# Performance work log

Measured on AMD Instinct MI355X. Metric: run time of the kernel, lower is better.

The kernel has to match this reference:

```python
import jax, jax.numpy as jnp
import numpy as np
import math

B, N, DEG, C, F0, NCLS = 128, 512, 8, 128, 128, 10
E = B * N * DEG
RATIO = 0.8
K1 = math.ceil(RATIO * N)    # 410
K2 = math.ceil(RATIO * K1)   # 328
K3 = math.ceil(RATIO * K2)   # 263


def setup_inputs() -> dict:
    key = jax.random.key(0)
    ks = jax.random.split(key, 32)
    x = jax.random.normal(ks[0], (B * N, F0), jnp.float32)
    epg = N * DEG
    src_l = jax.random.randint(ks[1], (B, epg), 0, N)
    dst_l = jax.random.randint(ks[2], (B, epg), 0, N)
    off = (jnp.arange(B, dtype=jnp.int32) * N)[:, None]
    edge_src = (src_l + off).reshape(-1).astype(jnp.int32)
    edge_dst = (dst_l + off).reshape(-1).astype(jnp.int32)

    def lin(k, fi, fo):
        return jax.random.normal(k, (fi, fo), jnp.float32) / np.float32(np.sqrt(fi))

    inp = {"x": x, "edge_src": edge_src, "edge_dst": edge_dst}
    i = 3
    for s, fi in (("1", F0), ("2", C), ("3", C)):
        inp["Wroot" + s] = lin(ks[i], fi, C); i += 1
        inp["Wrel" + s] = lin(ks[i], fi, C); i += 1
        inp["brel" + s] = jnp.zeros((C,), jnp.float32)
        inp["p" + s] = jax.random.normal(ks[i], (C,), jnp.float32); i += 1
    inp["W1"] = lin(ks[i], 2 * C, 128); i += 1
    inp["b1"] = jnp.zeros((128,), jnp.float32)
    inp["W2"] = lin(ks[i], 128, 64); i += 1
    inp["b2"] = jnp.zeros((64,), jnp.float32)
    inp["W3"] = lin(ks[i], 64, NCLS); i += 1
    inp["b3"] = jnp.zeros((NCLS,), jnp.float32)
    return inp


def graph_conv(x, src, dst, emask, Wroot, Wrel, brel, num_nodes):
    # PyG GraphConv (aggr='add'): lin_rel(sum_j x_j) + lin_root(x_i)
    msg = x[src] * emask[:, None]                      # masked gather  [E, C]
    agg = jax.ops.segment_sum(msg, dst, num_segments=num_nodes)
    return agg @ Wrel + brel + x @ Wroot


def topk_pool(x, p, src, dst, emask, b, n, k):
    # score = tanh(x . p / ||p||), keep top-k nodes per graph, scale kept x by score
    score = jnp.tanh((x @ p) / jnp.linalg.norm(p))     # [b*n]
    vals, idx = jax.lax.top_k(score.reshape(b, n), k)  # [b, k]
    perm = (idx + (jnp.arange(b, dtype=idx.dtype) * n)[:, None]).reshape(-1)
    x_new = x[perm] * vals.reshape(-1, 1)
    inv = jnp.full((b * n,), -1, jnp.int32).at[perm].set(
        jnp.arange(b * k, dtype=jnp.int32))
    ns, nd = inv[src], inv[dst]
    nmask = emask * (ns >= 0) * (nd >= 0)
    return x_new, jnp.maximum(ns, 0), jnp.maximum(nd, 0), nmask


def readout(h, b, k):
    hb = h.reshape(b, k, -1)
    return jnp.concatenate([hb.max(axis=1), hb.mean(axis=1)], axis=-1)  # gmp||gap


def reference(x, edge_src, edge_dst,
              Wroot1, Wrel1, brel1, p1,
              Wroot2, Wrel2, brel2, p2,
              Wroot3, Wrel3, brel3, p3,
              W1, b1, W2, b2, W3, b3):
    emask = jnp.ones((E,), x.dtype)
    s, d = edge_src, edge_dst

    h = jax.nn.relu(graph_conv(x, s, d, emask, Wroot1, Wrel1, brel1, B * N))
    h, s, d, emask = topk_pool(h, p1, s, d, emask, B, N, K1)
    x1 = readout(h, B, K1)

    h = jax.nn.relu(graph_conv(h, s, d, emask, Wroot2, Wrel2, brel2, B * K1))
    h, s, d, emask = topk_pool(h, p2, s, d, emask, B, K1, K2)
    x2 = readout(h, B, K2)

    h = jax.nn.relu(graph_conv(h, s, d, emask, Wroot3, Wrel3, brel3, B * K2))
    h, s, d, emask = topk_pool(h, p3, s, d, emask, B, K2, K3)
    x3 = readout(h, B, K3)

    g = x1 + x2 + x3                                   # [B, 256]
    g = jax.nn.relu(g @ W1 + b1)                       # dropout is identity in eval
    g = jax.nn.relu(g @ W2 + b2)
    return jax.nn.log_softmax(g @ W3 + b3, axis=-1)    # [B, NCLS]
```

## Files before the change

### kernel.cpp

```cpp
#include <hip/hip_runtime.h>
#include <hip/hip_bf16.h>
#include <math.h>

#define B_G   128
#define N0    512
#define DEG   8
#define CCH   128
#define EPG   (N0*DEG)
#define E_TOTAL (B_G*EPG)
#define K1    410
#define K2    328
#define K3    263
#define NCLS  10

#define SWZ(row, cb) ((((cb) ^ ((row) & 7)) << 2))

using bf16x8 = __attribute__((ext_vector_type(8))) __bf16;
using f32x4  = __attribute__((ext_vector_type(4))) float;
typedef unsigned short ushort;
typedef unsigned int uint;
typedef unsigned long long u64;

__device__ __forceinline__ ushort f2b(float f) {
    uint u = __float_as_uint(f);
    u += 0x7fffu + ((u >> 16) & 1u);
    return (ushort)(u >> 16);
}
__device__ __forceinline__ float b2f(ushort h) {
    return __uint_as_float(((uint)h) << 16);
}
__device__ __forceinline__ void split2(float v, ushort& hi, ushort& lo) {
    hi = f2b(v);
    lo = f2b(v - b2f(hi));
}
__device__ __forceinline__ uint pksplit(float v) {
    ushort h, l; split2(v, h, l);
    return (uint)h | ((uint)l << 16);
}
__device__ __forceinline__ float unpk(uint u) {
    return __uint_as_float(u << 16) + __uint_as_float(u & 0xffff0000u);
}
__device__ __forceinline__ float keyval(u64 key) {
    uint tu = (uint)(key >> 32);
    uint su = (tu & 0x80000000u) ? (tu & 0x7fffffffu) : ~tu;
    return __uint_as_float(su);
}

__global__ __launch_bounds__(512) void setup_kernel(
        const float* __restrict__ Wrel0, const float* __restrict__ Wroot0,
        const float* __restrict__ Wrel1, const float* __restrict__ Wroot1,
        const float* __restrict__ Wrel2, const float* __restrict__ Wroot2,
        ushort* __restrict__ Bph, ushort* __restrict__ Bpl,
        const int* __restrict__ es, const int* __restrict__ ed,
        int* __restrict__ indptr0, int* __restrict__ counts0, ushort* __restrict__ srclist0) {
    __shared__ uint epk[EPG];
    __shared__ int cnt[512], pref[512], curs[512];
    if (blockIdx.x < B_G) {
        int b = blockIdx.x, tid = threadIdx.x;
        cnt[tid] = 0;
        __syncthreads();
        int base = b * EPG;
        for (int i = tid; i < EPG; i += 512) {
            int s = es[base + i] & (N0 - 1);
            int d = ed[base + i] & (N0 - 1);
            epk[i] = (uint)s | ((uint)d << 16);
            atomicAdd(&cnt[d], 1);
        }
        __syncthreads();
        pref[tid] = cnt[tid];
        __syncthreads();
        for (int off = 1; off < 512; off <<= 1) {
            int v = (tid >= off) ? pref[tid - off] : 0;
            __syncthreads();
            pref[tid] += v;
            __syncthreads();
        }
        int excl = tid ? pref[tid - 1] : 0;
        indptr0[b * N0 + tid] = base + excl;
        counts0[b * N0 + tid] = cnt[tid];
        curs[tid] = excl;
        __syncthreads();
        for (int i = tid; i < EPG; i += 512) {
            uint wv = epk[i];
            int dl = wv >> 16;
            int pos = atomicAdd(&curs[dl], 1);
            srclist0[base + pos] = (ushort)(wv & 0xFFFFu);
        }
    } else {
        int i = (blockIdx.x - B_G) * 512 + threadIdx.x;
        if (i < 3 * 32768) {
            int layer = i >> 15, rem = i & 32767;
            int j = rem & 7, lane = (rem >> 3) & 63, cf = (rem >> 9) & 7, ks = rem >> 12;
            int k = ks * 32 + (lane >> 4) * 8 + j;
            int c = cf * 16 + (lane & 15);
            const float* Wrel  = layer == 0 ? Wrel0  : layer == 1 ? Wrel1  : Wrel2;
            const float* Wroot = layer == 0 ? Wroot0 : layer == 1 ? Wroot1 : Wroot2;
            float v = (k < 128) ? Wrel[k * 128 + c] : Wroot[(k - 128) * 128 + c];
            ushort hi, lo; split2(v, hi, lo);
            Bph[i] = hi; Bpl[i] = lo;
        }
    }
}

__global__ __launch_bounds__(1024) void aggregate0(
        const float* __restrict__ xf,
        const int* __restrict__ indptr, const int* __restrict__ counts,
        const ushort* __restrict__ srclist,
        uint* __restrict__ aggp) {
    extern __shared__ float slab[];
    int b = blockIdx.x >> 2, q = blockIdx.x & 3;
    int tid = threadIdx.x;
    const float4* xf4 = (const float4*)xf;
    for (int t = tid; t < N0 * 8; t += 1024) {
        int nd = t >> 3, c4 = t & 7;
        float4 u = xf4[(size_t)(b * N0 + nd) * 32 + q * 8 + c4];
        *(float4*)&slab[nd * 32 + SWZ(nd, c4)] = u;
    }
    __syncthreads();
    int wave = tid >> 6, lane = tid & 63;
    int gl = lane >> 3, sub = lane & 7;
    for (int g = wave; g < N0 / 8; g += 16) {
        int d = g * 8 + gl;
        int beg = indptr[b * N0 + d];
        int cnt = counts[b * N0 + d];
        float4 acc = make_float4(0.f, 0.f, 0.f, 0.f);
        int id_next = (cnt > 0) ? (int)srclist[beg] : 0;
        for (int j = 0; j < cnt; j++) {
            int id = id_next;
            if (j + 1 < cnt) id_next = (int)srclist[beg + j + 1];
            const float4 v = *(const float4*)&slab[id * 32 + SWZ(id, sub)];
            acc.x += v.x; acc.y += v.y; acc.z += v.z; acc.w += v.w;
        }
        uint4 o;
        o.x = pksplit(acc.x); o.y = pksplit(acc.y);
        o.z = pksplit(acc.z); o.w = pksplit(acc.w);
        *(uint4*)&aggp[(size_t)(b * N0 + d) * CCH + q * 32 + sub * 4] = o;
    }
}

__global__ __launch_bounds__(512, 4) void transform_mfma(
        const uint* __restrict__ aggp, const uint* __restrict__ rootp,
        const float* __restrict__ rootf,
        const ushort* __restrict__ Bph, const ushort* __restrict__ Bpl,
        const float* __restrict__ brel, const float* __restrict__ pvec,
        uint* __restrict__ hout, float* __restrict__ score) {
    __shared__ ushort ldsBh[16384];
    __shared__ ushort ldsBl[16384];
    int tid = threadIdx.x;
    int wave = tid >> 6, lane = tid & 63;
    int r = lane & 15, kb = lane >> 4;
    int rows0 = blockIdx.x * 128 + wave * 16;
    int gid = rows0 + r;

    f32x4 acc[8];
#pragma unroll
    for (int cf = 0; cf < 8; cf++) acc[cf] = (f32x4)(0.f);

    union U16 { uint u[4]; bf16x8 v; };

#pragma unroll
    for (int half = 0; half < 2; half++) {
        if (half) __syncthreads();
#pragma unroll
        for (int i = 0; i < 4; i++) {
            int idx = tid + i * 512;
            ((uint4*)ldsBh)[idx] = ((const uint4*)(Bph + half * 16384))[idx];
            ((uint4*)ldsBl)[idx] = ((const uint4*)(Bpl + half * 16384))[idx];
        }
        __syncthreads();
#pragma unroll
        for (int ks4 = 0; ks4 < 4; ks4++) {
            U16 ah, al;
            if (half && rootf) {
                const float* R = rootf + (size_t)gid * CCH + ks4 * 32 + kb * 8;
                float4 f0 = *(const float4*)R;
                float4 f1 = *(const float4*)(R + 4);
                float c[8] = {f0.x, f0.y, f0.z, f0.w, f1.x, f1.y, f1.z, f1.w};
#pragma unroll
                for (int p2 = 0; p2 < 4; p2++) {
                    ushort h0, l0, h1, l1;
                    split2(c[2 * p2], h0, l0);
                    split2(c[2 * p2 + 1], h1, l1);
                    ah.u[p2] = (uint)h0 | ((uint)h1 << 16);
                    al.u[p2] = (uint)l0 | ((uint)l1 << 16);
                }
            } else {
                const uint* A = half ? rootp : aggp;
                size_t rowbase = (size_t)gid * CCH + ks4 * 32 + kb * 8;
                uint4 ua = *(const uint4*)&A[rowbase];
                uint4 ub = *(const uint4*)&A[rowbase + 4];
                ah.u[0] = (ua.x & 0xffffu) | (ua.y << 16);
                ah.u[1] = (ua.z & 0xffffu) | (ua.w << 16);
                ah.u[2] = (ub.x & 0xffffu) | (ub.y << 16);
                ah.u[3] = (ub.z & 0xffffu) | (ub.w << 16);
                al.u[0] = (ua.x >> 16) | (ua.y & 0xffff0000u);
                al.u[1] = (ua.z >> 16) | (ua.w & 0xffff0000u);
                al.u[2] = (ub.x >> 16) | (ub.y & 0xffff0000u);
                al.u[3] = (ub.z >> 16) | (ub.w & 0xffff0000u);
            }
#pragma unroll
            for (int cf = 0; cf < 8; cf++) {
                bf16x8 bh = *(const bf16x8*)&ldsBh[((ks4 * 8 + cf) * 64 + lane) * 8];
                bf16x8 bl = *(const bf16x8*)&ldsBl[((ks4 * 8 + cf) * 64 + lane) * 8];
                acc[cf] = __builtin_amdgcn_mfma_f32_16x16x32_bf16(ah.v, bl, acc[cf], 0, 0, 0);
                acc[cf] = __builtin_amdgcn_mfma_f32_16x16x32_bf16(al.v, bh, acc[cf], 0, 0, 0);
                acc[cf] = __builtin_amdgcn_mfma_f32_16x16x32_bf16(ah.v, bh, acc[cf], 0, 0, 0);
            }
        }
    }

    float pv[8], bb[8], q = 0.f;
#pragma unroll
    for (int cf = 0; cf < 8; cf++) {
        pv[cf] = pvec[cf * 16 + r];
        bb[cf] = brel[cf * 16 + r];
        q += pv[cf] * pv[cf];
    }
    float dots[4] = {0.f, 0.f, 0.f, 0.f};
#pragma unroll
    for (int cf = 0; cf < 8; cf++) {
#pragma unroll
        for (int reg = 0; reg < 4; reg++) {
            float v = acc[cf][reg] + bb[cf];
            v = v > 0.f ? v : 0.f;
            hout[(size_t)(rows0 + kb * 4 + reg) * CCH + cf * 16 + r] = pksplit(v);
            dots[reg] += v * pv[cf];
        }
    }
#pragma unroll
    for (int off = 1; off < 16; off <<= 1) {
        q += __shfl_xor(q, off);
#pragma unroll
        for (int reg = 0; reg < 4; reg++) dots[reg] += __shfl_xor(dots[reg], off);
    }
    if (r == 0) {
        float inv_norm = rsqrtf(q);
#pragma unroll
        for (int reg = 0; reg < 4; reg++)
            score[rows0 + kb * 4 + reg] = tanhf(dots[reg] * inv_norm);
    }
}

__global__ __launch_bounds__(1024) void pool_kernel(
        const float* __restrict__ score, const uint* __restrict__ hp,
        float* __restrict__ gpart,
        const int* __restrict__ ipt_in, const int* __restrict__ cnt_in,
        const ushort* __restrict__ src_in,
        int* __restrict__ ipt_out, int* __restrict__ cnt_out,
        ushort* __restrict__ src_out,
        uint* __restrict__ pooledX, uint* __restrict__ aggout,
        int n, int k, int do_next) {
    int b = blockIdx.x >> 2, q = blockIdx.x & 3;
    int tid = threadIdx.x;
    __shared__ short invl[512];
    __shared__ short old_of[512];
    __shared__ float sval[512];
    __shared__ int hist[256];
    __shared__ int cum[257];
    __shared__ int bc[1];
    __shared__ float redbuf[1024];
    __shared__ int prefL[512];
    __shared__ int wtot[8], woff[8];
    extern __shared__ float slab[];

    u64 key = 0ull;
    bool has = (tid < n);
    if (has) {
        uint u = __float_as_uint(score[b * n + tid]);
        u = (u & 0x80000000u) ? ~u : (u | 0x80000000u);
        key = ((u64)u << 32) | (uint)(~tid);
        sval[tid] = keyval(key);
    }
    for (int t = tid; t < n * 8; t += 1024) {
        int nd = t >> 3, c4 = t & 7;
        uint4 u = *(const uint4*)&hp[(size_t)(b * n + nd) * CCH + q * 32 + c4 * 4];
        *(float4*)&slab[nd * 32 + SWZ(nd, c4)] =
            make_float4(unpk(u.x), unpk(u.y), unpk(u.z), unpk(u.w));
    }
    bool active = has, sure = false;
    int rem = k;
    for (int pass = 0; pass < 8; pass++) {
        int dig = (int)((key >> (56 - 8 * pass)) & 255);
        if (tid < 256) hist[tid] = 0;
        __syncthreads();
        if (active) atomicAdd(&hist[dig], 1);
        __syncthreads();
        if (tid < 64) {
            int b0 = hist[tid * 4], b1 = hist[tid * 4 + 1];
            int b2 = hist[tid * 4 + 2], b3 = hist[tid * 4 + 3];
            int s = b0 + b1 + b2 + b3;
            int suf = s;
#pragma unroll
            for (int o = 1; o < 64; o <<= 1) {
                int t2 = __shfl_down(suf, o);
                if (tid + o < 64) suf += t2;
            }
            int after = suf - s;
            cum[tid * 4 + 3] = after + b3;
            cum[tid * 4 + 2] = after + b3 + b2;
            cum[tid * 4 + 1] = after + b3 + b2 + b1;
            cum[tid * 4 + 0] = after + s;
            if (tid == 0) cum[256] = 0;
        }
        __syncthreads();
        if (tid < 256 && cum[tid] >= rem && cum[tid + 1] < rem) bc[0] = tid;
        __syncthreads();
        int dstar = bc[0];
        int hcnt = hist[dstar];
        rem -= cum[dstar + 1];
        if (active) {
            if (dig > dstar) { sure = true; active = false; }
            else if (dig < dstar) active = false;
        }
        __syncthreads();
        if (hcnt == 1) break;
    }
    bool sel = sure || (active && rem > 0);
    {
        int lane = tid & 63;
        int v = sel ? 1 : 0;
        int incl = v;
#pragma unroll
        for (int o = 1; o < 64; o <<= 1) {
            int t2 = __shfl_up(incl, o);
            if (lane >= o) incl += t2;
        }
        if (tid < 512 && lane == 63) wtot[tid >> 6] = incl;
        __syncthreads();
        if (tid < 8) {
            int s = 0;
            for (int w = 0; w < tid; w++) s += wtot[w];
            woff[tid] = s;
        }
        __syncthreads();
        if (tid < 512) {
            int rank = incl - v + woff[tid >> 6];
            invl[tid] = sel ? (short)rank : (short)-1;
            if (sel) old_of[rank] = (short)tid;
        }
        __syncthreads();
    }
    for (int t = tid; t < n * 8; t += 1024) {
        int nd = t >> 3, c4 = t & 7;
        if (invl[nd] >= 0) {
            float v = sval[nd];
            float* p = &slab[nd * 32 + SWZ(nd, c4)];
            p[0] *= v; p[1] *= v; p[2] *= v; p[3] *= v;
        }
    }
    __syncthreads();
    if (tid < 512) {
        int w = tid >> 5, ch = tid & 31;
        int cb = ch >> 2, ce = ch & 3;
        float mx = -1e30f, sm = 0.f;
        for (int nd = w; nd < n; nd += 16) {
            float v = slab[nd * 32 + SWZ(nd, cb) + ce];
            if (invl[nd] >= 0) { mx = fmaxf(mx, v); sm += v; }
        }
        redbuf[w * 32 + ch] = mx;
        redbuf[512 + w * 32 + ch] = sm;
    }
    __syncthreads();
    if (tid < 32) {
        float m = -1e30f, s = 0.f;
        for (int w = 0; w < 16; w++) {
            m = fmaxf(m, redbuf[w * 32 + tid]);
            s += redbuf[512 + w * 32 + tid];
        }
        gpart[b * 256 + q * 32 + tid] = m;
        gpart[b * 256 + 128 + q * 32 + tid] = s / (float)k;
    }
    if (!do_next) return;
    for (int t = tid; t < k * 8; t += 1024) {
        int rank = t >> 3, c4 = t & 7;
        int old = (int)old_of[rank];
        const float* p = &slab[old * 32 + SWZ(old, c4)];
        uint4 o;
        o.x = pksplit(p[0]); o.y = pksplit(p[1]);
        o.z = pksplit(p[2]); o.w = pksplit(p[3]);
        *(uint4*)&pooledX[(size_t)(b * k + rank) * CCH + q * 32 + c4 * 4] = o;
    }
    {
        int wave = tid >> 6, lane = tid & 63;
        int gl = lane >> 3, sub = lane & 7;
        int ngroups = (k + 7) >> 3;
        for (int g = wave; g < ngroups; g += 16) {
            int d = g * 8 + gl;
            bool act = d < k;
            int beg = 0, cc = 0;
            if (act) {
                int old = (int)old_of[d];
                beg = ipt_in[b * n + old];
                cc = cnt_in[b * n + old];
            }
            float4 acc = make_float4(0.f, 0.f, 0.f, 0.f);
            int s_next = (cc > 0) ? (int)src_in[beg] : 0;
            for (int j = 0; j < cc; j++) {
                int s = s_next;
                if (j + 1 < cc) s_next = (int)src_in[beg + j + 1];
                if (invl[s] >= 0) {
                    const float4 v = *(const float4*)&slab[s * 32 + SWZ(s, sub)];
                    acc.x += v.x; acc.y += v.y; acc.z += v.z; acc.w += v.w;
                }
            }
            if (act) {
                uint4 o;
                o.x = pksplit(acc.x); o.y = pksplit(acc.y);
                o.z = pksplit(acc.z); o.w = pksplit(acc.w);
                *(uint4*)&aggout[(size_t)(b * k + d) * CCH + q * 32 + sub * 4] = o;
            }
        }
    }
    if (q == 0) {
        int beg = 0, c = 0, nk = 0;
        if (tid < k) {
            int old = (int)old_of[tid];
            beg = ipt_in[b * n + old];
            c = cnt_in[b * n + old];
            for (int t = 0; t < c; t++)
                if (invl[src_in[beg + t]] >= 0) nk++;
        }
        int lane = tid & 63;
        int incl = (tid < 512 && tid < k) ? nk : 0;
#pragma unroll
        for (int o = 1; o < 64; o <<= 1) {
            int t2 = __shfl_up(incl, o);
            if (lane >= o) incl += t2;
        }
        if (tid < 512 && lane == 63) wtot[tid >> 6] = incl;
        __syncthreads();
        if (tid < 8) {
            int s = 0;
            for (int w = 0; w < tid; w++) s += wtot[w];
            woff[tid] = s;
        }
        __syncthreads();
        if (tid < 512) prefL[tid] = incl + woff[tid >> 6];
        __syncthreads();
        if (tid < k) {
            int excl = tid ? prefL[tid - 1] : 0;
            ipt_out[b * k + tid] = b * EPG + excl;
            cnt_out[b * k + tid] = nk;
            int pos = b * EPG + excl;
            for (int t = 0; t < c; t++) {
                int ns = invl[src_in[beg + t]];
                if (ns >= 0) src_out[pos++] = (ushort)ns;
            }
        }
    }
}

__global__ __launch_bounds__(128) void mlp_kernel(const float* __restrict__ gpart,
        const float* __restrict__ W1, const float* __restrict__ b1,
        const float* __restrict__ W2, const float* __restrict__ b2,
        const float* __restrict__ W3, const float* __restrict__ b3,
        float* __restrict__ out) {
    int b = blockIdx.x, t = threadIdx.x;
    __shared__ float gs[256], h1[128], h2[64], lg[10];
    const float* g0 = gpart + ((size_t)0 * B_G + b) * 256;
    const float* g1 = gpart + ((size_t)1 * B_G + b) * 256;
    const float* g2 = gpart + ((size_t)2 * B_G + b) * 256;
    gs[t] = g0[t] + g1[t] + g2[t];
    gs[128 + t] = g0[128 + t] + g1[128 + t] + g2[128 + t];
    __syncthreads();
    {
        float a = b1[t];
        for (int c = 0; c < 256; c++) a += gs[c] * W1[c * 128 + t];
        h1[t] = fmaxf(a, 0.f);
    }
    __syncthreads();
    if (t < 64) {
        float a = b2[t];
        for (int c = 0; c < 128; c++) a += h1[c] * W2[c * 64 + t];
        h2[t] = fmaxf(a, 0.f);
    }
    __syncthreads();
    if (t < 10) {
        float a = b3[t];
        for (int c = 0; c < 64; c++) a += h2[c] * W3[c * 10 + t];
        lg[t] = a;
    }
    __syncthreads();
    if (t < 10) {
        float m = lg[0];
        for (int i = 1; i < 10; i++) m = fmaxf(m, lg[i]);
        float s = 0.f;
        for (int i = 0; i < 10; i++) s += expf(lg[i] - m);
        out[b * 10 + t] = lg[t] - m - logf(s);
    }
}

extern "C" void kernel_launch(void* const* d_in, const int* in_sizes, int n_in,
                              void* d_out, int out_size, void* d_ws, size_t ws_size,
                              hipStream_t stream) {
    (void)in_sizes; (void)n_in; (void)out_size; (void)ws_size;
    const float* x0 = (const float*)d_in[0];
    const int* es = (const int*)d_in[1];
    const int* ed = (const int*)d_in[2];
    const float* Wroot[3] = {(const float*)d_in[3], (const float*)d_in[7], (const float*)d_in[11]};
    const float* Wrel[3]  = {(const float*)d_in[4], (const float*)d_in[8], (const float*)d_in[12]};
    const float* brel[3]  = {(const float*)d_in[5], (const float*)d_in[9], (const float*)d_in[13]};
    const float* pvec[3]  = {(const float*)d_in[6], (const float*)d_in[10], (const float*)d_in[14]};
    const float* W1 = (const float*)d_in[15];
    const float* b1 = (const float*)d_in[16];
    const float* W2 = (const float*)d_in[17];
    const float* b2 = (const float*)d_in[18];
    const float* W3 = (const float*)d_in[19];
    const float* b3 = (const float*)d_in[20];

    size_t off = 0;
    char* base = (char*)d_ws;
    auto alloc = [&](size_t bytes) -> void* {
        void* p = base + off;
        off += (bytes + 255) & ~(size_t)255;
        return p;
    };
    const size_t FEATP = (size_t)(B_G * N0) * CCH * 4;
    uint* P0 = (uint*)alloc(FEATP);
    uint* P1 = (uint*)alloc(FEATP);
    uint* P2 = (uint*)alloc(FEATP);
    ushort* Bph = (ushort*)alloc((size_t)3 * 32768 * 2);
    ushort* Bpl = (ushort*)alloc((size_t)3 * 32768 * 2);
    int* iptA = (int*)alloc((size_t)(B_G * N0) * 4);
    int* cntA = (int*)alloc((size_t)(B_G * N0) * 4);
    ushort* srcA = (ushort*)alloc((size_t)E_TOTAL * 2);
    int* iptB = (int*)alloc((size_t)(B_G * N0) * 4);
    int* cntB = (int*)alloc((size_t)(B_G * N0) * 4);
    ushort* srcB = (ushort*)alloc((size_t)E_TOTAL * 2);
    float* score = (float*)alloc((size_t)(B_G * N0) * 4);
    float* gpart = (float*)alloc((size_t)3 * B_G * 256 * 4);

    setup_kernel<<<B_G + (3 * 32768 + 511) / 512, 512, 0, stream>>>(
        Wrel[0], Wroot[0], Wrel[1], Wroot[1], Wrel[2], Wroot[2],
        Bph, Bpl, es, ed, iptA, cntA, srcA);

    aggregate0<<<4 * B_G, 1024, (size_t)N0 * 32 * 4, stream>>>(
        x0, iptA, cntA, srcA, P1);
    transform_mfma<<<B_G * N0 / 128, 512, 0, stream>>>(
        P1, nullptr, x0, Bph, Bpl, brel[0], pvec[0], P0, score);
    pool_kernel<<<4 * B_G, 1024, (size_t)N0 * 32 * 4, stream>>>(
        score, P0, gpart + (size_t)0 * B_G * 256,
        iptA, cntA, srcA, iptB, cntB, srcB, P2, P1, N0, K1, 1);

    transform_mfma<<<B_G * K1 / 128, 512, 0, stream>>>(
        P1, P2, nullptr, Bph + 32768, Bpl + 32768, brel[1], pvec[1], P0, score);
    pool_kernel<<<4 * B_G, 1024, (size_t)K1 * 32 * 4, stream>>>(
        score, P0, gpart + (size_t)1 * B_G * 256,
        iptB, cntB, srcB, iptA, cntA, srcA, P2, P1, K1, K2, 1);

    transform_mfma<<<B_G * K2 / 128, 512, 0, stream>>>(
        P1, P2, nullptr, Bph + 2 * 32768, Bpl + 2 * 32768, brel[2], pvec[2], P0, score);
    pool_kernel<<<4 * B_G, 1024, (size_t)K2 * 32 * 4, stream>>>(
        score, P0, gpart + (size_t)2 * B_G * 256,
        iptA, cntA, srcA, nullptr, nullptr, nullptr, nullptr, nullptr, K2, K3, 0);

    mlp_kernel<<<B_G, 128, 0, stream>>>(gpart, W1, b1, W2, b2, W3, b3, (float*)d_out);
}
```

Measured before the change: 199.6 us.

## Replace per-stage graph compaction with validity masks over the fixed node layout

After: 194.2 us (median of 2 runs). 2.7% less time.

```diff
diff --git a/kernel.cpp b/kernel.cpp
--- a/kernel.cpp
+++ b/kernel.cpp
@@ -242,42 +242,41 @@
 }
 
 __global__ __launch_bounds__(1024) void pool_kernel(
-        const float* __restrict__ score, const uint* __restrict__ hp,
+        const float* __restrict__ score, uint* __restrict__ hp,
         float* __restrict__ gpart,
-        const int* __restrict__ ipt_in, const int* __restrict__ cnt_in,
-        const ushort* __restrict__ src_in,
-        int* __restrict__ ipt_out, int* __restrict__ cnt_out,
-        ushort* __restrict__ src_out,
-        uint* __restrict__ pooledX, uint* __restrict__ aggout,
-        int n, int k, int do_next) {
+        const int* __restrict__ ipt, const int* __restrict__ cnt,
+        const ushort* __restrict__ srcl,
+        const int* __restrict__ valid_in,
+        int* __restrict__ valid_out,
+        uint* __restrict__ aggout,
+        int k) {
     int b = blockIdx.x >> 2, q = blockIdx.x & 3;
     int tid = threadIdx.x;
-    __shared__ short invl[512];
-    __shared__ short old_of[512];
+    __shared__ char selm[512];
     __shared__ float sval[512];
     __shared__ int hist[256];
     __shared__ int cum[257];
     __shared__ int bc[1];
-    __shared__ float redbuf[1024];
-    __shared__ int prefL[512];
-    __shared__ int wtot[8], woff[8];
+    __shared__ float redbuf[2048];
     extern __shared__ float slab[];
 
     u64 key = 0ull;
-    bool has = (tid < n);
-    if (has) {
-        uint u = __float_as_uint(score[b * n + tid]);
-        u = (u & 0x80000000u) ? ~u : (u | 0x80000000u);
-        key = ((u64)u << 32) | (uint)(~tid);
-        sval[tid] = keyval(key);
-    }
-    for (int t = tid; t < n * 8; t += 1024) {
+    if (tid < 512) {
+        bool v = (!valid_in) || (valid_in[b * N0 + tid] != 0);
+        if (v) {
+            uint u = __float_as_uint(score[b * N0 + tid]);
+            u = (u & 0x80000000u) ? ~u : (u | 0x80000000u);
+            key = ((u64)u << 32) | (uint)(~tid);
+            sval[tid] = keyval(key);
+        }
+    }
+    for (int t = tid; t < N0 * 8; t += 1024) {
         int nd = t >> 3, c4 = t & 7;
-        uint4 u = *(const uint4*)&hp[(size_t)(b * n + nd) * CCH + q * 32 + c4 * 4];
+        uint4 u = *(const uint4*)&hp[(size_t)(b * N0 + nd) * CCH + q * 32 + c4 * 4];
         *(float4*)&slab[nd * 32 + SWZ(nd, c4)] =
             make_float4(unpk(u.x), unpk(u.y), unpk(u.z), unpk(u.w));
     }
-    bool active = has, sure = false;
+    bool active = (tid < 512) && (key != 0ull), sure = false;
     int rem = k;
     for (int pass = 0; pass < 8; pass++) {
         int dig = (int)((key >> (56 - 8 * pass)) & 255);
@@ -316,89 +315,61 @@
         if (hcnt == 1) break;
     }
     bool sel = sure || (active && rem > 0);
-    {
-        int lane = tid & 63;
-        int v = sel ? 1 : 0;
-        int incl = v;
-#pragma unroll
-        for (int o = 1; o < 64; o <<= 1) {
-            int t2 = __shfl_up(incl, o);
-            if (lane >= o) incl += t2;
-        }
-        if (tid < 512 && lane == 63) wtot[tid >> 6] = incl;
-        __syncthreads();
-        if (tid < 8) {
-            int s = 0;
-            for (int w = 0; w < tid; w++) s += wtot[w];
-            woff[tid] = s;
-        }
-        __syncthreads();
-        if (tid < 512) {
-            int rank = incl - v + woff[tid >> 6];
-            invl[tid] = sel ? (short)rank : (short)-1;
-            if (sel) old_of[rank] = (short)tid;
-        }
-        __syncthreads();
-    }
-    for (int t = tid; t < n * 8; t += 1024) {
+    if (tid < 512) selm[tid] = sel ? 1 : 0;
+    __syncthreads();
+    for (int t = tid; t < N0 * 8; t += 1024) {
         int nd = t >> 3, c4 = t & 7;
-        if (invl[nd] >= 0) {
+        if (selm[nd]) {
             float v = sval[nd];
             float* p = &slab[nd * 32 + SWZ(nd, c4)];
-            p[0] *= v; p[1] *= v; p[2] *= v; p[3] *= v;
-        }
-    }
-    __syncthreads();
-    if (tid < 512) {
+            float a0 = p[0] * v, a1 = p[1] * v, a2 = p[2] * v, a3 = p[3] * v;
+            p[0] = a0; p[1] = a1; p[2] = a2; p[3] = a3;
+            if (valid_out) {
+                uint4 o;
+                o.x = pksplit(a0); o.y = pksplit(a1);
+                o.z = pksplit(a2); o.w = pksplit(a3);
+                *(uint4*)&hp[(size_t)(b * N0 + nd) * CCH + q * 32 + c4 * 4] = o;
+            }
+        }
+    }
+    __syncthreads();
+    {
         int w = tid >> 5, ch = tid & 31;
         int cb = ch >> 2, ce = ch & 3;
         float mx = -1e30f, sm = 0.f;
-        for (int nd = w; nd < n; nd += 16) {
+        for (int nd = w; nd < N0; nd += 32) {
             float v = slab[nd * 32 + SWZ(nd, cb) + ce];
-            if (invl[nd] >= 0) { mx = fmaxf(mx, v); sm += v; }
+            if (selm[nd]) { mx = fmaxf(mx, v); sm += v; }
         }
         redbuf[w * 32 + ch] = mx;
-        redbuf[512 + w * 32 + ch] = sm;
+        redbuf[1024 + w * 32 + ch] = sm;
     }
     __syncthreads();
     if (tid < 32) {
         float m = -1e30f, s = 0.f;
-        for (int w = 0; w < 16; w++) {
+        for (int w = 0; w < 32; w++) {
             m = fmaxf(m, redbuf[w * 32 + tid]);
-            s += redbuf[512 + w * 32 + tid];
+            s += redbuf[1024 + w * 32 + tid];
         }
         gpart[b * 256 + q * 32 + tid] = m;
         gpart[b * 256 + 128 + q * 32 + tid] = s / (float)k;
     }
-    if (!do_next) return;
-    for (int t = tid; t < k * 8; t += 1024) {
-        int rank = t >> 3, c4 = t & 7;
-        int old = (int)old_of[rank];
-        const float* p = &slab[old * 32 + SWZ(old, c4)];
-        uint4 o;
-        o.x = pksplit(p[0]); o.y = pksplit(p[1]);
-        o.z = pksplit(p[2]); o.w = pksplit(p[3]);
-        *(uint4*)&pooledX[(size_t)(b * k + rank) * CCH + q * 32 + c4 * 4] = o;
-    }
+    if (!valid_out) return;
+    if (q == 0 && tid < 512) valid_out[b * N0 + tid] = selm[tid] ? 1 : 0;
     {
         int wave = tid >> 6, lane = tid & 63;
         int gl = lane >> 3, sub = lane & 7;
-        int ngroups = (k + 7) >> 3;
-        for (int g = wave; g < ngroups; g += 16) {
+        for (int g = wave; g < N0 / 8; g += 16) {
             int d = g * 8 + gl;
-            bool act = d < k;
+            bool act = selm[d] != 0;
             int beg = 0, cc = 0;
-            if (act) {
-                int old = (int)old_of[d];
-                beg = ipt_in[b * n + old];
-                cc = cnt_in[b * n + old];
-            }
+            if (act) { beg = ipt[b * N0 + d]; cc = cnt[b * N0 + d]; }
             float4 acc = make_float4(0.f, 0.f, 0.f, 0.f);
-            int s_next = (cc > 0) ? (int)src_in[beg] : 0;
+            int s_next = (cc > 0) ? (int)srcl[beg] : 0;
             for (int j = 0; j < cc; j++) {
                 int s = s_next;
-                if (j + 1 < cc) s_next = (int)src_in[beg + j + 1];
-                if (invl[s] >= 0) {
+                if (j + 1 < cc) s_next = (int)srcl[beg + j + 1];
+                if (selm[s]) {
                     const float4 v = *(const float4*)&slab[s * 32 + SWZ(s, sub)];
                     acc.x += v.x; acc.y += v.y; acc.z += v.z; acc.w += v.w;
                 }
@@ -407,44 +378,7 @@
                 uint4 o;
                 o.x = pksplit(acc.x); o.y = pksplit(acc.y);
                 o.z = pksplit(acc.z); o.w = pksplit(acc.w);
-                *(uint4*)&aggout[(size_t)(b * k + d) * CCH + q * 32 + sub * 4] = o;
-            }
-        }
-    }
-    if (q == 0) {
-        int beg = 0, c = 0, nk = 0;
-        if (tid < k) {
-            int old = (int)old_of[tid];
-            beg = ipt_in[b * n + old];
-            c = cnt_in[b * n + old];
-            for (int t = 0; t < c; t++)
-                if (invl[src_in[beg + t]] >= 0) nk++;
-        }
-        int lane = tid & 63;
-        int incl = (tid < 512 && tid < k) ? nk : 0;
-#pragma unroll
-        for (int o = 1; o < 64; o <<= 1) {
-            int t2 = __shfl_up(incl, o);
-            if (lane >= o) incl += t2;
-        }
-        if (tid < 512 && lane == 63) wtot[tid >> 6] = incl;
-        __syncthreads();
-        if (tid < 8) {
-            int s = 0;
-            for (int w = 0; w < tid; w++) s += wtot[w];
-            woff[tid] = s;
-        }
-        __syncthreads();
-        if (tid < 512) prefL[tid] = incl + woff[tid >> 6];
-        __syncthreads();
-        if (tid < k) {
-            int excl = tid ? prefL[tid - 1] : 0;
-            ipt_out[b * k + tid] = b * EPG + excl;
-            cnt_out[b * k + tid] = nk;
-            int pos = b * EPG + excl;
-            for (int t = 0; t < c; t++) {
-                int ns = invl[src_in[beg + t]];
-                if (ns >= 0) src_out[pos++] = (ushort)ns;
+                *(uint4*)&aggout[(size_t)(b * N0 + d) * CCH + q * 32 + sub * 4] = o;
             }
         }
     }
@@ -516,43 +450,42 @@
         return p;
     };
     const size_t FEATP = (size_t)(B_G * N0) * CCH * 4;
-    uint* P0 = (uint*)alloc(FEATP);
+    uint* PA = (uint*)alloc(FEATP);
+    uint* PB = (uint*)alloc(FEATP);
     uint* P1 = (uint*)alloc(FEATP);
-    uint* P2 = (uint*)alloc(FEATP);
     ushort* Bph = (ushort*)alloc((size_t)3 * 32768 * 2);
     ushort* Bpl = (ushort*)alloc((size_t)3 * 32768 * 2);
-    int* iptA = (int*)alloc((size_t)(B_G * N0) * 4);
-    int* cntA = (int*)alloc((size_t)(B_G * N0) * 4);
-    ushort* srcA = (ushort*)alloc((size_t)E_TOTAL * 2);
-    int* iptB = (int*)alloc((size_t)(B_G * N0) * 4);
-    int* cntB = (int*)alloc((size_t)(B_G * N0) * 4);
-    ushort* srcB = (ushort*)alloc((size_t)E_TOTAL * 2);
+    int* ipt = (int*)alloc((size_t)(B_G * N0) * 4);
+    int* cnt = (int*)alloc((size_t)(B_G * N0) * 4);
+    ushort* srcl = (ushort*)alloc((size_t)E_TOTAL * 2);
+    int* valid1 = (int*)alloc((size_t)(B_G * N0) * 4);
+    int* valid2 = (int*)alloc((size_t)(B_G * N0) * 4);
     float* score = (float*)alloc((size_t)(B_G * N0) * 4);
     float* gpart = (float*)alloc((size_t)3 * B_G * 256 * 4);
 
     setup_kernel<<<B_G + (3 * 32768 + 511) / 512, 512, 0, stream>>>(
         Wrel[0], Wroot[0], Wrel[1], Wroot[1], Wrel[2], Wroot[2],
-        Bph, Bpl, es, ed, iptA, cntA, srcA);
-
-    aggregate0<<<4 * B_G, 1024, (size_t)N0 * 32 * 4, stream>>>(
-        x0, iptA, cntA, srcA, P1);
+        Bph, Bpl, es, ed, ipt, cnt, srcl);
+
+    const size_t SLAB = (size_t)N0 * 32 * 4;
+    aggregate0<<<4 * B_G, 1024, SLAB, stream>>>(x0, ipt, cnt, srcl, P1);
     transform_mfma<<<B_G * N0 / 128, 512, 0, stream>>>(
-        P1, nullptr, x0, Bph, Bpl, brel[0], pvec[0], P0, score);
-    pool_kernel<<<4 * B_G, 1024, (size_t)N0 * 32 * 4, stream>>>(
-        score, P0, gpart + (size_t)0 * B_G * 256,
-        iptA, cntA, srcA, iptB, cntB, srcB, P2, P1, N0, K1, 1);
-
-    transform_mfma<<<B_G * K1 / 128, 512, 0, stream>>>(
-        P1, P2, nullptr, Bph + 32768, Bpl + 32768, brel[1], pvec[1], P0, score);
-    pool_kernel<<<4 * B_G, 1024, (size_t)K1 * 32 * 4, stream>>>(
-        score, P0, gpart + (size_t)1 * B_G * 256,
-        iptB, cntB, srcB, iptA, cntA, srcA, P2, P1, K1, K2, 1);
-
-    transform_mfma<<<B_G * K2 / 128, 512, 0, stream>>>(
-        P1, P2, nullptr, Bph + 2 * 32768, Bpl + 2 * 32768, brel[2], pvec[2], P0, score);
-    pool_kernel<<<4 * B_G, 1024, (size_t)K2 * 32 * 4, stream>>>(
-        score, P0, gpart + (size_t)2 * B_G * 256,
-        iptA, cntA, srcA, nullptr, nullptr, nullptr, nullptr, nullptr, K2, K3, 0);
+        P1, nullptr, x0, Bph, Bpl, brel[0], pvec[0], PA, score);
+    pool_kernel<<<4 * B_G, 1024, SLAB, stream>>>(
+        score, PA, gpart + (size_t)0 * B_G * 256,
+        ipt, cnt, srcl, nullptr, valid1, P1, K1);
+
+    transform_mfma<<<B_G * N0 / 128, 512, 0, stream>>>(
+        P1, PA, nullptr, Bph + 32768, Bpl + 32768, brel[1], pvec[1], PB, score);
+    pool_kernel<<<4 * B_G, 1024, SLAB, stream>>>(
+        score, PB, gpart + (size_t)1 * B_G * 256,
+        ipt, cnt, srcl, valid1, valid2, P1, K2);
+
+    transform_mfma<<<B_G * N0 / 128, 512, 0, stream>>>(
+        P1, PB, nullptr, Bph + 2 * 32768, Bpl + 2 * 32768, brel[2], pvec[2], PA, score);
+    pool_kernel<<<4 * B_G, 1024, SLAB, stream>>>(
+        score, PA, gpart + (size_t)2 * B_G * 256,
+        ipt, cnt, srcl, valid2, nullptr, nullptr, K3);
 
     mlp_kernel<<<B_G, 128, 0, stream>>>(gpart, W1, b1, W2, b2, W3, b3, (float*)d_out);
 }
```
